# Optimization experiments

Hardware: AMD Instinct MI355X
Metric: run time of the kernel (lower is better)

## Reference

```python
import jax, jax.numpy as jnp
import numpy as np
from jax import lax

B, T, H, W, E = 64, 8, 8, 8, 512
REC = 2048


def setup_inputs() -> dict:
    key = jax.random.key(0)
    kx, kwi, kwr = jax.random.split(key, 3)
    x = jax.random.normal(kx, (B, T, H, W, E), dtype=jnp.float32)
    W_input = jax.random.normal(kwi, (E, REC), dtype=jnp.float32) / np.sqrt(E)
    W_recurrent = jax.random.normal(kwr, (REC, REC), dtype=jnp.float32) / np.sqrt(REC)
    return {"x": x, "W_input": W_input, "W_recurrent": W_recurrent}


def reference(x, W_input, W_recurrent):
    b, t, h, w, e = x.shape
    R = t * h * w
    rec = W_recurrent.shape[0]
    k = int(rec * 0.4)  # 819, matches torch: int(recurrent_size * 0.4)
    x_seq = jnp.swapaxes(x.reshape(b, R, e), 0, 1)  # [R, B, E]
    row_idx = jnp.arange(b)[:, None]

    def step(r, inp):
        z = r @ W_recurrent                    # [B, REC]
        vals, idx = lax.top_k(z, k)            # [B, k]
        s = jnp.zeros_like(z).at[row_idx, idx].set(vals)  # scatter top-k back
        r_new = jnp.tanh(inp @ W_input + s)
        r_new = r_new / (jnp.linalg.norm(r_new, axis=-1, keepdims=True) + 1e-6)
        return r_new, None

    r0 = jnp.zeros((b, rec), dtype=x.dtype)
    r_final, _ = lax.scan(step, r0, x_seq)
    return r_final
```

## Files before the change

kernel.cpp:

```cpp
#include <hip/hip_runtime.h>

#define NSTEP 512
#define EDIM  512
#define REC   2048
#define NB    64
#define KSEL  819
#define KC    8
#define ZCH   256
#define AP    264
#define CSTR  16896

typedef unsigned short u16;
typedef __bf16 bf16x8 __attribute__((ext_vector_type(8)));
typedef float  f32x4  __attribute__((ext_vector_type(4)));
typedef unsigned long long ull;

static __device__ __forceinline__ f32x4 mfma16(bf16x8 a, bf16x8 b, f32x4 c) {
    return __builtin_amdgcn_mfma_f32_16x16x32_bf16(a, b, c, 0, 0, 0);
}

static __device__ __forceinline__ void split2(float v, u16& c0, u16& c1) {
    __bf16 b0 = (__bf16)v;
    __bf16 b1 = (__bf16)(v - (float)b0);
    c0 = __builtin_bit_cast(u16, b0);
    c1 = __builtin_bit_cast(u16, b1);
}

static __device__ __forceinline__ void cstore4f(float* p, float v) {
    __hip_atomic_store((unsigned*)p, __float_as_uint(v), __ATOMIC_RELAXED, __HIP_MEMORY_SCOPE_AGENT);
}
static __device__ __forceinline__ void cstore4u(unsigned* p, unsigned v) {
    __hip_atomic_store(p, v, __ATOMIC_RELAXED, __HIP_MEMORY_SCOPE_AGENT);
}
static __device__ __forceinline__ unsigned cload4u(const unsigned* p) {
    return __hip_atomic_load(p, __ATOMIC_RELAXED, __HIP_MEMORY_SCOPE_AGENT);
}
static __device__ __forceinline__ void cstore8u(void* p, ull v) {
    __hip_atomic_store((ull*)p, v, __ATOMIC_RELAXED, __HIP_MEMORY_SCOPE_AGENT);
}
static __device__ __forceinline__ ull cload8u(const void* p) {
    return __hip_atomic_load((const ull*)p, __ATOMIC_RELAXED, __HIP_MEMORY_SCOPE_AGENT);
}
static __device__ __forceinline__ float2 cload8f(const float* p) {
    ull u = cload8u(p);
    float2 v; __builtin_memcpy(&v, &u, 8);
    return v;
}

__device__ __forceinline__ void gbarA(unsigned* bar, int bid, int tid,
                                      unsigned gen, bool wait)
{
    __syncthreads();
    if (tid == 0) cstore4u(&bar[bid], gen);
    if (bid == 0 && tid < 64) {
        const ull* sl = (const ull*)bar;
        for (;;) {
            const ull v0 = cload8u(&sl[tid * 2]);
            const ull v1 = cload8u(&sl[tid * 2 + 1]);
            const bool ok = ((unsigned)v0 >= gen) && ((unsigned)(v0 >> 32) >= gen)
                         && ((unsigned)v1 >= gen) && ((unsigned)(v1 >> 32) >= gen);
            if (__all(ok)) break;
            __builtin_amdgcn_s_sleep(1);
        }
        if (tid < 16) cstore4u(&bar[1024 + tid * 32], gen);
    }
    if (wait) {
        if (tid == 0) {
            const int g = bid >> 4;
            while (cload4u(&bar[1024 + g * 32]) < gen)
                __builtin_amdgcn_s_sleep(1);
            __asm__ volatile("" ::: "memory");
        }
        __syncthreads();
    }
}

__device__ __forceinline__ void gbarB(unsigned* bar, int bid, int tid, unsigned gen)
{
    __syncthreads();
    if (bid < NB && tid == 0) cstore4u(&bar[512 + bid], gen);
    if (bid == 0 && tid < 64) {
        for (;;) {
            const unsigned v = cload4u(&bar[512 + tid]);
            if (__all(v >= gen)) break;
            __builtin_amdgcn_s_sleep(1);
        }
        if (tid < 16) cstore4u(&bar[1536 + tid * 32], gen);
    }
    if (tid == 0) {
        const int g = bid >> 4;
        while (cload4u(&bar[1536 + g * 32]) < gen)
            __builtin_amdgcn_s_sleep(1);
        __asm__ volatile("" ::: "memory");
    }
    __syncthreads();
}

__global__ __launch_bounds__(512, 1)
void rnn_persistent(const float* __restrict__ x, const float* __restrict__ Wi,
                    const float* __restrict__ Wr, float* __restrict__ out,
                    u16* __restrict__ rTu, float* __restrict__ zb,
                    u16* __restrict__ Ybf, unsigned* __restrict__ bar)
{
    extern __shared__ __align__(16) char smem[];
    u16* WrSu = (u16*)smem;
    u16* aSu  = (u16*)(smem + 67584);
    float* WiP = (float*)smem;
    float* xP  = (float*)(smem + 16384);
    unsigned*      kS    = (unsigned*)(smem + 67584);
    unsigned char* selS  = (unsigned char*)(smem + 67584 + 8192);
    unsigned*      hist  = (unsigned*)(smem + 67584 + 10240);
    __shared__ unsigned s_byte, s_newrem, s_cnteq;
    __shared__ float red[8];

    const int bid = blockIdx.x;
    const int tid = threadIdx.x;
    const int kc = bid & 7, nc = bid >> 3;
    const int n0 = nc * 64, kcbase = kc * ZCH;
    const int wid = tid >> 6, lane = tid & 63;
    const int q = lane >> 4, l16 = lane & 15;
    const int Moff = (wid & 3) * 16, Npair = wid >> 2;
    const bool isB = (bid < NB);

    {
        const int t0 = bid * 2;
        const int tr4 = (tid >> 5) * 4;
        const int tc4 = (tid & 31) * 4;
        for (int nc2 = 0; nc2 < 16; ++nc2) {
            const int n0y = nc2 * 128;
            f32x4 acc[2][4];
#pragma unroll
            for (int h = 0; h < 2; ++h)
#pragma unroll
                for (int i = 0; i < 4; ++i) acc[h][i] = (f32x4){0,0,0,0};
            for (int kr = 0; kr < 16; ++kr) {
                const int k0y = kr * 32;
                __syncthreads();
                {
                    const int col4 = (tid & 31) * 4, row = tid >> 5;
                    *(float4*)&WiP[row * 128 + col4] =
                        *(const float4*)(Wi + (long long)(k0y + row) * REC + n0y + col4);
                    *(float4*)&WiP[(row + 16) * 128 + col4] =
                        *(const float4*)(Wi + (long long)(k0y + row + 16) * REC + n0y + col4);
                }
                for (int h = 0; h < 2; ++h) {
                    __syncthreads();
                    {
                        const int b = tid & 63, e4 = (tid >> 6) * 4;
                        const float4 v = *(const float4*)(x + ((long long)b * NSTEP + (t0 + h)) * EDIM + k0y + e4);
                        xP[(e4    ) * 64 + b] = v.x;
                        xP[(e4 + 1) * 64 + b] = v.y;
                        xP[(e4 + 2) * 64 + b] = v.z;
                        xP[(e4 + 3) * 64 + b] = v.w;
                    }
                    __syncthreads();
#pragma unroll 8
                    for (int kk = 0; kk < 32; ++kk) {
                        const float4 af = *(const float4*)&xP[kk * 64 + tr4];
                        const float4 bf = *(const float4*)&WiP[kk * 128 + tc4];
                        const float av[4] = {af.x, af.y, af.z, af.w};
#pragma unroll
                        for (int i = 0; i < 4; ++i) {
                            acc[h][i].x += av[i] * bf.x;
                            acc[h][i].y += av[i] * bf.y;
                            acc[h][i].z += av[i] * bf.z;
                            acc[h][i].w += av[i] * bf.w;
                        }
                    }
                }
            }
#pragma unroll
            for (int h = 0; h < 2; ++h)
#pragma unroll
                for (int i = 0; i < 4; ++i) {
                    const long long yrow = (long long)(t0 + h) * 64 + tr4 + i;
                    u16 o[4];
                    o[0] = __builtin_bit_cast(u16, (__bf16)acc[h][i].x);
                    o[1] = __builtin_bit_cast(u16, (__bf16)acc[h][i].y);
                    o[2] = __builtin_bit_cast(u16, (__bf16)acc[h][i].z);
                    o[3] = __builtin_bit_cast(u16, (__bf16)acc[h][i].w);
                    ull pk; __builtin_memcpy(&pk, o, 8);
                    cstore8u(&Ybf[yrow * REC + n0y + tc4], pk);
                }
        }
    }
    {
        const int g = bid * 512 + tid;
        if (g < 65536) cstore8u(rTu + (long long)g * 4, 0ull);
        cstore4f(zb + g, 0.f);
    }
    gbarA(bar, bid, tid, 1u, true);

    {
        for (int it = 0; it < 32; ++it) {
            const int row = it * 8 + wid;
            const int col = lane;
            const float v = Wr[(long long)(kcbase + row) * REC + n0 + col];
            u16 s0, s1; split2(v, s0, s1);
            const int base = col * AP + row;
            WrSu[base] = s0;
            WrSu[CSTR + base] = s1;
        }
        __syncthreads();
    }

    const int hw = tid >> 5, hl = tid & 31;
    for (int t = 0; t < NSTEP; ++t) {
        float* zcur = zb + (size_t)(t & 1) * 131072;
        float* znxt = zb + (size_t)((t + 1) & 1) * 131072;
        cstore4f(znxt + bid * 512 + tid, 0.f);
        {
            ull va[8], vbv[8];
#pragma unroll
            for (int i = 0; i < 8; ++i) {
                const int c = i >> 2;
                const int b = (i & 3) * 16 + hw;
                const u16* src = rTu + (long long)c * 131072 + (long long)b * REC + kcbase + hl * 8;
                va[i] = cload8u(src);
                vbv[i] = cload8u(src + 4);
            }
#pragma unroll
            for (int i = 0; i < 8; ++i) {
                const int c = i >> 2;
                const int b = (i & 3) * 16 + hw;
                u16* dst = aSu + c * CSTR + b * AP + hl * 8;
                *(ull*)dst = va[i];
                *(ull*)(dst + 4) = vbv[i];
            }
        }
        __syncthreads();

        f32x4 acc0 = {0,0,0,0}, acc1 = {0,0,0,0};
#pragma unroll
        for (int ks = 0; ks < 8; ++ks) {
            const int kk = ks * 32 + q * 8;
            const u16* ap = aSu + (Moff + l16) * AP + kk;
            bf16x8 A0 = *(const bf16x8*)(ap);
            bf16x8 A1 = *(const bf16x8*)(ap + CSTR);
            const u16* bp0 = WrSu + (Npair * 32 + l16) * AP + kk;
            bf16x8 B00 = *(const bf16x8*)(bp0);
            bf16x8 B01 = *(const bf16x8*)(bp0 + CSTR);
            const u16* bp1 = bp0 + 16 * AP;
            bf16x8 B10 = *(const bf16x8*)(bp1);
            bf16x8 B11 = *(const bf16x8*)(bp1 + CSTR);
            acc0 = mfma16(A0, B00, acc0);
            acc1 = mfma16(A0, B10, acc1);
            acc0 = mfma16(A0, B01, acc0);
            acc1 = mfma16(A0, B11, acc1);
            acc0 = mfma16(A1, B00, acc0);
            acc1 = mfma16(A1, B10, acc1);
        }
        {
            const int colA = n0 + Npair * 32 + l16;
#pragma unroll
            for (int i = 0; i < 4; ++i) {
                float* zp = zcur + (long long)(Moff + q * 4 + i) * REC + colA;
                unsafeAtomicAdd(zp,      ((float*)&acc0)[i]);
                unsafeAtomicAdd(zp + 16, ((float*)&acc1)[i]);
            }
        }
        gbarA(bar, bid, tid, (unsigned)(t + 2), isB);

        if (isB) {
            const int b = bid;
            const int j0 = tid * 4;
            float zs[4];
            {
                const float2 u0 = cload8f(zcur + (long long)b * REC + j0);
                const float2 u1 = cload8f(zcur + (long long)b * REC + j0 + 2);
                zs[0] = u0.x; zs[1] = u0.y; zs[2] = u1.x; zs[3] = u1.y;
            }
            const ushort4 yv = *(const ushort4*)&Ybf[((long long)t * 64 + b) * REC + j0];
            unsigned kv[4];
#pragma unroll
            for (int s = 0; s < 4; ++s) {
                const unsigned u = __float_as_uint(zs[s]);
                kv[s] = (u & 0x80000000u) ? ~u : (u | 0x80000000u);
            }
            unsigned* hw_ = hist + wid * 256;
            unsigned prefix = 0, remaining = KSEL;
            int done = 0;
            for (int byte = 3; byte >= 0 && !done; --byte) {
                {
                    uint4 zz = {0u, 0u, 0u, 0u};
                    *(uint4*)&hw_[lane * 4] = zz;
                }
                const int shift = byte * 8;
                const unsigned pmask = (byte == 3) ? 0u : (0xFFFFFFFFu << (shift + 8));
#pragma unroll
                for (int s = 0; s < 4; ++s) {
                    if ((kv[s] & pmask) == prefix)
                        atomicAdd(&hw_[(kv[s] >> shift) & 255u], 1u);
                }
                __syncthreads();
                if (tid < 64) {
                    unsigned c0 = 0, c1 = 0, c2 = 0, c3 = 0;
#pragma unroll
                    for (int w = 0; w < 8; ++w) {
                        const uint4 hv = *(const uint4*)&hist[w * 256 + tid * 4];
                        c0 += hv.x; c1 += hv.y; c2 += hv.z; c3 += hv.w;
                    }
                    const unsigned tot = c0 + c1 + c2 + c3;
                    unsigned suf = tot;
#pragma unroll
                    for (int st = 1; st < 64; st <<= 1) {
                        unsigned o = __shfl_down(suf, (unsigned)st);
                        if (tid + st >= 64) o = 0u;
                        suf += o;
                    }
                    unsigned S[5];
                    S[0] = suf; S[1] = suf - c0; S[2] = suf - c0 - c1;
                    S[3] = suf - c0 - c1 - c2; S[4] = suf - tot;
                    const unsigned cc[4] = {c0, c1, c2, c3};
#pragma unroll
                    for (int qq = 0; qq < 4; ++qq) {
                        if (S[qq] >= remaining && S[qq + 1] < remaining) {
                            s_byte = (unsigned)(tid * 4 + qq);
                            s_newrem = remaining - S[qq + 1];
                            s_cnteq = cc[qq];
                        }
                    }
                }
                __syncthreads();
                prefix |= (s_byte << shift);
                remaining = s_newrem;
                if (remaining == s_cnteq) done = 1;
            }
            unsigned char sel[4];
            if (done) {
#pragma unroll
                for (int s = 0; s < 4; ++s)
                    sel[s] = (kv[s] >= prefix) ? 1 : 0;
            } else {
                *(uint4*)&kS[j0] = *(uint4*)kv;
                __syncthreads();
                if (tid == 0) {
                    unsigned rem = remaining;
                    const unsigned T = prefix;
                    for (int j = 0; j < REC; ++j) {
                        const unsigned k = kS[j];
                        unsigned char sl = 0;
                        if (k > T) sl = 1;
                        else if (k == T && rem > 0u) { sl = 1; --rem; }
                        selS[j] = sl;
                    }
                }
                __syncthreads();
#pragma unroll
                for (int s = 0; s < 4; ++s) sel[s] = selS[j0 + s];
            }
            float rn[4]; float ss = 0.f;
            const u16 ya[4] = {yv.x, yv.y, yv.z, yv.w};
#pragma unroll
            for (int s = 0; s < 4; ++s) {
                const float y = __uint_as_float(((unsigned)ya[s]) << 16);
                const float v = y + (sel[s] ? zs[s] : 0.f);
                const float th = tanhf(v);
                rn[s] = th; ss += th * th;
            }
#pragma unroll
            for (int off = 32; off > 0; off >>= 1)
                ss += __shfl_down(ss, (unsigned)off);
            if (lane == 0) red[wid] = ss;
            __syncthreads();
            float a = 0.f;
#pragma unroll
            for (int i = 0; i < 8; ++i) a += red[i];
            const float inv = 1.0f / (sqrtf(a) + 1e-6f);
            u16 o0[4], o1[4];
            float4 ov;
#pragma unroll
            for (int s = 0; s < 4; ++s) {
                const float v = rn[s] * inv;
                split2(v, o0[s], o1[s]);
                ((float*)&ov)[s] = v;
            }
            ull p0, p1;
            __builtin_memcpy(&p0, o0, 8); __builtin_memcpy(&p1, o1, 8);
            cstore8u(rTu + (long long)b * REC + j0, p0);
            cstore8u(rTu + 131072 + (long long)b * REC + j0, p1);
            if (t == NSTEP - 1)
                *(float4*)&out[(long long)b * REC + j0] = ov;
        }
        gbarB(bar, bid, tid, (unsigned)(t + 1));
    }
}

extern "C" void kernel_launch(void* const* d_in, const int* in_sizes, int n_in,
                              void* d_out, int out_size, void* d_ws, size_t ws_size,
                              hipStream_t stream)
{
    const float* x   = (const float*)d_in[0];
    const float* Win = (const float*)d_in[1];
    const float* Wr  = (const float*)d_in[2];
    float* out = (float*)d_out;

    char* ws = (char*)d_ws;
    const size_t BAR = 8192;
    unsigned* bar = (unsigned*)ws;
    float* zb  = (float*)(ws + BAR);
    u16*   rTu = (u16*)(ws + BAR + 2 * 524288);
    u16*   Ybf = (u16*)(ws + BAR + 2 * 524288 + 524288);

    static int smem_set = 0;
    if (!smem_set) {
        hipFuncSetAttribute((const void*)rnn_persistent,
                            hipFuncAttributeMaxDynamicSharedMemorySize, 135168);
        smem_set = 1;
    }
    hipMemsetAsync(bar, 0, BAR, stream);
    rnn_persistent<<<256, 512, 135168, stream>>>(x, Win, Wr, out, rTu, zb, Ybf, bar);
}
```

Baseline: 7.594 ms.

## Use MFMA for input projection, flatten grid barriers, ballot-based top byte histogram

Computes the x@W_input prologue with split-bf16 MFMA instead of scalar FP32 FMAs, after first transposing and splitting W_input into a workspace buffer. The two-level hierarchical grid barriers are replaced by flat barriers in which every block polls all arrival flags directly. The Ybf load is issued before the barrier wait so its latency overlaps the wait. The first radix histogram pass uses wave ballots instead of LDS atomics. The extra prologue barrier and transpose add setup cost, and the flat polling puts more traffic on the barrier flags.

After: 10.21 ms. 34.5% more time.

```diff
diff --git a/kernel.cpp b/kernel.cpp
--- a/kernel.cpp
+++ b/kernel.cpp
@@ -9,6 +9,7 @@
 #define ZCH   256
 #define AP    264
 #define CSTR  16896
+#define WITC  1048576
 
 typedef unsigned short u16;
 typedef __bf16 bf16x8 __attribute__((ext_vector_type(8)));
@@ -47,66 +48,17 @@
     return v;
 }
 
-__device__ __forceinline__ void gbarA(unsigned* bar, int bid, int tid,
-                                      unsigned gen, bool wait)
-{
-    __syncthreads();
-    if (tid == 0) cstore4u(&bar[bid], gen);
-    if (bid == 0 && tid < 64) {
-        const ull* sl = (const ull*)bar;
-        for (;;) {
-            const ull v0 = cload8u(&sl[tid * 2]);
-            const ull v1 = cload8u(&sl[tid * 2 + 1]);
-            const bool ok = ((unsigned)v0 >= gen) && ((unsigned)(v0 >> 32) >= gen)
-                         && ((unsigned)v1 >= gen) && ((unsigned)(v1 >> 32) >= gen);
-            if (__all(ok)) break;
-            __builtin_amdgcn_s_sleep(1);
-        }
-        if (tid < 16) cstore4u(&bar[1024 + tid * 32], gen);
-    }
-    if (wait) {
-        if (tid == 0) {
-            const int g = bid >> 4;
-            while (cload4u(&bar[1024 + g * 32]) < gen)
-                __builtin_amdgcn_s_sleep(1);
-            __asm__ volatile("" ::: "memory");
-        }
-        __syncthreads();
-    }
-}
-
-__device__ __forceinline__ void gbarB(unsigned* bar, int bid, int tid, unsigned gen)
-{
-    __syncthreads();
-    if (bid < NB && tid == 0) cstore4u(&bar[512 + bid], gen);
-    if (bid == 0 && tid < 64) {
-        for (;;) {
-            const unsigned v = cload4u(&bar[512 + tid]);
-            if (__all(v >= gen)) break;
-            __builtin_amdgcn_s_sleep(1);
-        }
-        if (tid < 16) cstore4u(&bar[1536 + tid * 32], gen);
-    }
-    if (tid == 0) {
-        const int g = bid >> 4;
-        while (cload4u(&bar[1536 + g * 32]) < gen)
-            __builtin_amdgcn_s_sleep(1);
-        __asm__ volatile("" ::: "memory");
-    }
-    __syncthreads();
-}
-
 __global__ __launch_bounds__(512, 1)
 void rnn_persistent(const float* __restrict__ x, const float* __restrict__ Wi,
                     const float* __restrict__ Wr, float* __restrict__ out,
                     u16* __restrict__ rTu, float* __restrict__ zb,
-                    u16* __restrict__ Ybf, unsigned* __restrict__ bar)
+                    u16* __restrict__ Ybf, u16* __restrict__ WiTu,
+                    unsigned* __restrict__ bar)
 {
     extern __shared__ __align__(16) char smem[];
     u16* WrSu = (u16*)smem;
     u16* aSu  = (u16*)(smem + 67584);
-    float* WiP = (float*)smem;
-    float* xP  = (float*)(smem + 16384);
+    float* tp = (float*)smem;
     unsigned*      kS    = (unsigned*)(smem + 67584);
     unsigned char* selS  = (unsigned char*)(smem + 67584 + 8192);
     unsigned*      hist  = (unsigned*)(smem + 67584 + 10240);
@@ -123,64 +75,113 @@
     const bool isB = (bid < NB);
 
     {
+        const int jt = bid & 31, et = bid >> 5;
+        const int j0 = jt * 64, e0 = et * 64;
+        const int rr = tid >> 6, ln = tid & 63;
+#pragma unroll
+        for (int k = 0; k < 8; ++k) {
+            const int r = k * 8 + rr;
+            tp[r * 65 + ln] = Wi[(long long)(e0 + r) * REC + j0 + ln];
+        }
+        __syncthreads();
+        const int c = tid >> 3, e8 = (tid & 7) * 8;
+        u16 h[8], l[8];
+#pragma unroll
+        for (int i = 0; i < 8; ++i) split2(tp[(e8 + i) * 65 + c], h[i], l[i]);
+        ull ph0, ph1, pl0, pl1;
+        __builtin_memcpy(&ph0, &h[0], 8); __builtin_memcpy(&ph1, &h[4], 8);
+        __builtin_memcpy(&pl0, &l[0], 8); __builtin_memcpy(&pl1, &l[4], 8);
+        const long long bI = (long long)(j0 + c) * 512 + e0 + e8;
+        cstore8u(&WiTu[bI], ph0);        cstore8u(&WiTu[bI + 4], ph1);
+        cstore8u(&WiTu[WITC + bI], pl0); cstore8u(&WiTu[WITC + bI + 4], pl1);
+    }
+    __syncthreads();
+    if (tid == 0) cstore4u(&bar[bid], 1u);
+    if (tid < 256) { while (cload4u(&bar[tid]) < 1u) __builtin_amdgcn_s_sleep(1); }
+    __asm__ volatile("" ::: "memory");
+    __syncthreads();
+
+    {
         const int t0 = bid * 2;
-        const int tr4 = (tid >> 5) * 4;
-        const int tc4 = (tid & 31) * 4;
-        for (int nc2 = 0; nc2 < 16; ++nc2) {
-            const int n0y = nc2 * 128;
-            f32x4 acc[2][4];
-#pragma unroll
-            for (int h = 0; h < 2; ++h)
-#pragma unroll
-                for (int i = 0; i < 4; ++i) acc[h][i] = (f32x4){0,0,0,0};
-            for (int kr = 0; kr < 16; ++kr) {
-                const int k0y = kr * 32;
+        for (int jc = 0; jc < 32; ++jc) {
+            const int j0y = jc * 64;
+            f32x4 aY[2][2];
+#pragma unroll
+            for (int tt = 0; tt < 2; ++tt)
+#pragma unroll
+                for (int i = 0; i < 2; ++i) aY[tt][i] = (f32x4){0,0,0,0};
+            for (int kc2 = 0; kc2 < 2; ++kc2) {
                 __syncthreads();
-                {
-                    const int col4 = (tid & 31) * 4, row = tid >> 5;
-                    *(float4*)&WiP[row * 128 + col4] =
-                        *(const float4*)(Wi + (long long)(k0y + row) * REC + n0y + col4);
-                    *(float4*)&WiP[(row + 16) * 128 + col4] =
-                        *(const float4*)(Wi + (long long)(k0y + row + 16) * REC + n0y + col4);
-                }
-                for (int h = 0; h < 2; ++h) {
+#pragma unroll
+                for (int i = 0; i < 8; ++i) {
+                    const int chunk = i * 512 + tid;
+                    const int cc = chunk >> 11;
+                    const int jj = (chunk & 2047) >> 5;
+                    const int e8 = chunk & 31;
+                    const u16* src = WiTu + (long long)cc * WITC
+                                   + (long long)(j0y + jj) * 512 + kc2 * 256 + e8 * 8;
+                    const ull w0 = *(const ull*)src;
+                    const ull w1 = *(const ull*)(src + 4);
+                    u16* dst = WrSu + cc * CSTR + jj * AP + e8 * 8;
+                    *(ull*)dst = w0;
+                    *(ull*)(dst + 4) = w1;
+                }
+#pragma unroll
+                for (int tt = 0; tt < 2; ++tt) {
                     __syncthreads();
-                    {
-                        const int b = tid & 63, e4 = (tid >> 6) * 4;
-                        const float4 v = *(const float4*)(x + ((long long)b * NSTEP + (t0 + h)) * EDIM + k0y + e4);
-                        xP[(e4    ) * 64 + b] = v.x;
-                        xP[(e4 + 1) * 64 + b] = v.y;
-                        xP[(e4 + 2) * 64 + b] = v.z;
-                        xP[(e4 + 3) * 64 + b] = v.w;
+#pragma unroll
+                    for (int it = 0; it < 8; ++it) {
+                        const int b = it * 8 + wid;
+                        const float4 v = *(const float4*)(x
+                            + ((long long)b * NSTEP + (t0 + tt)) * EDIM
+                            + kc2 * 256 + lane * 4);
+                        u16 hh[4], ll[4];
+                        split2(v.x, hh[0], ll[0]); split2(v.y, hh[1], ll[1]);
+                        split2(v.z, hh[2], ll[2]); split2(v.w, hh[3], ll[3]);
+                        ull ph, pl;
+                        __builtin_memcpy(&ph, hh, 8); __builtin_memcpy(&pl, ll, 8);
+                        *(ull*)&aSu[b * AP + lane * 4] = ph;
+                        *(ull*)&aSu[CSTR + b * AP + lane * 4] = pl;
                     }
                     __syncthreads();
-#pragma unroll 8
-                    for (int kk = 0; kk < 32; ++kk) {
-                        const float4 af = *(const float4*)&xP[kk * 64 + tr4];
-                        const float4 bf = *(const float4*)&WiP[kk * 128 + tc4];
-                        const float av[4] = {af.x, af.y, af.z, af.w};
-#pragma unroll
-                        for (int i = 0; i < 4; ++i) {
-                            acc[h][i].x += av[i] * bf.x;
-                            acc[h][i].y += av[i] * bf.y;
-                            acc[h][i].z += av[i] * bf.z;
-                            acc[h][i].w += av[i] * bf.w;
-                        }
-                    }
-                }
-            }
-#pragma unroll
-            for (int h = 0; h < 2; ++h)
+                    f32x4 a0 = aY[tt][0], a1 = aY[tt][1];
+#pragma unroll
+                    for (int ks = 0; ks < 8; ++ks) {
+                        const int kk = ks * 32 + q * 8;
+                        const u16* ap = aSu + (Moff + l16) * AP + kk;
+                        bf16x8 A0 = *(const bf16x8*)(ap);
+                        bf16x8 A1 = *(const bf16x8*)(ap + CSTR);
+                        const u16* bp0 = WrSu + (Npair * 32 + l16) * AP + kk;
+                        bf16x8 B00 = *(const bf16x8*)(bp0);
+                        bf16x8 B01 = *(const bf16x8*)(bp0 + CSTR);
+                        const u16* bp1 = bp0 + 16 * AP;
+                        bf16x8 B10 = *(const bf16x8*)(bp1);
+                        bf16x8 B11 = *(const bf16x8*)(bp1 + CSTR);
+                        a0 = mfma16(A0, B00, a0);
+                        a1 = mfma16(A0, B10, a1);
+                        a0 = mfma16(A0, B01, a0);
+                        a1 = mfma16(A0, B11, a1);
+                        a0 = mfma16(A1, B00, a0);
+                        a1 = mfma16(A1, B10, a1);
+                    }
+                    aY[tt][0] = a0; aY[tt][1] = a1;
+                }
+            }
+            const int jb = j0y + Npair * 32 + l16;
+#pragma unroll
+            for (int tt = 0; tt < 2; ++tt)
 #pragma unroll
                 for (int i = 0; i < 4; ++i) {
-                    const long long yrow = (long long)(t0 + h) * 64 + tr4 + i;
-                    u16 o[4];
-                    o[0] = __builtin_bit_cast(u16, (__bf16)acc[h][i].x);
-                    o[1] = __builtin_bit_cast(u16, (__bf16)acc[h][i].y);
-                    o[2] = __builtin_bit_cast(u16, (__bf16)acc[h][i].z);
-                    o[3] = __builtin_bit_cast(u16, (__bf16)acc[h][i].w);
-                    ull pk; __builtin_memcpy(&pk, o, 8);
-                    cstore8u(&Ybf[yrow * REC + n0y + tc4], pk);
+                    const int row = Moff + q * 4 + i;
+                    const unsigned w0 = (unsigned)__builtin_bit_cast(u16, (__bf16)((float*)&aY[tt][0])[i]);
+                    const unsigned w1 = (unsigned)__builtin_bit_cast(u16, (__bf16)((float*)&aY[tt][1])[i]);
+                    const unsigned o0 = (unsigned)__shfl_xor((int)w0, 1);
+                    const unsigned o1 = (unsigned)__shfl_xor((int)w1, 1);
+                    if ((lane & 1) == 0) {
+                        const long long yb = ((long long)(t0 + tt) * 64 + row) * REC + jb;
+                        cstore4u((unsigned*)&Ybf[yb],      w0 | (o0 << 16));
+                        cstore4u((unsigned*)&Ybf[yb + 16], w1 | (o1 << 16));
+                    }
                 }
         }
     }
@@ -189,7 +190,11 @@
         if (g < 65536) cstore8u(rTu + (long long)g * 4, 0ull);
         cstore4f(zb + g, 0.f);
     }
-    gbarA(bar, bid, tid, 1u, true);
+    __syncthreads();
+    if (tid == 0) cstore4u(&bar[bid], 2u);
+    if (tid < 256) { while (cload4u(&bar[tid]) < 2u) __builtin_amdgcn_s_sleep(1); }
+    __asm__ volatile("" ::: "memory");
+    __syncthreads();
 
     {
         for (int it = 0; it < 32; ++it) {
@@ -259,18 +264,25 @@
                 unsafeAtomicAdd(zp + 16, ((float*)&acc1)[i]);
             }
         }
-        gbarA(bar, bid, tid, (unsigned)(t + 2), isB);
+        __syncthreads();
+        if (tid == 0) cstore4u(&bar[bid], (unsigned)(t + 3));
 
         if (isB) {
             const int b = bid;
             const int j0 = tid * 4;
+            const ushort4 yv = *(const ushort4*)&Ybf[((long long)t * 64 + b) * REC + j0];
+            if (tid < 256) {
+                while (cload4u(&bar[tid]) < (unsigned)(t + 3)) __builtin_amdgcn_s_sleep(1);
+            }
+            __asm__ volatile("" ::: "memory");
+            __syncthreads();
+
             float zs[4];
             {
                 const float2 u0 = cload8f(zcur + (long long)b * REC + j0);
                 const float2 u1 = cload8f(zcur + (long long)b * REC + j0 + 2);
                 zs[0] = u0.x; zs[1] = u0.y; zs[2] = u1.x; zs[3] = u1.y;
             }
-            const ushort4 yv = *(const ushort4*)&Ybf[((long long)t * 64 + b) * REC + j0];
             unsigned kv[4];
 #pragma unroll
             for (int s = 0; s < 4; ++s) {
@@ -286,11 +298,28 @@
                     *(uint4*)&hw_[lane * 4] = zz;
                 }
                 const int shift = byte * 8;
-                const unsigned pmask = (byte == 3) ? 0u : (0xFFFFFFFFu << (shift + 8));
-#pragma unroll
-                for (int s = 0; s < 4; ++s) {
-                    if ((kv[s] & pmask) == prefix)
-                        atomicAdd(&hw_[(kv[s] >> shift) & 255u], 1u);
+                if (byte == 3) {
+                    unsigned bbs[4];
+#pragma unroll
+                    for (int s = 0; s < 4; ++s) bbs[s] = kv[s] >> 24;
+#pragma unroll
+                    for (int s = 0; s < 4; ++s) {
+                        ull rem = ~0ull;
+                        while (rem) {
+                            const int src = (int)__ffsll((unsigned long long)rem) - 1;
+                            const unsigned v = (unsigned)__shfl((int)bbs[s], src);
+                            const ull eq = __ballot(bbs[s] == v);
+                            if ((int)lane == src) hw_[v] += (unsigned)__popcll(eq);
+                            rem &= ~eq;
+                        }
+                    }
+                } else {
+                    const unsigned pmask = 0xFFFFFFFFu << (shift + 8);
+#pragma unroll
+                    for (int s = 0; s < 4; ++s) {
+                        if ((kv[s] & pmask) == prefix)
+                            atomicAdd(&hw_[(kv[s] >> shift) & 255u], 1u);
+                    }
                 }
                 __syncthreads();
                 if (tid < 64) {
@@ -382,7 +411,14 @@
             if (t == NSTEP - 1)
                 *(float4*)&out[(long long)b * REC + j0] = ov;
         }
-        gbarB(bar, bid, tid, (unsigned)(t + 1));
+
+        __syncthreads();
+        if (isB && tid == 0) cstore4u(&bar[512 + bid], (unsigned)(t + 1));
+        if (tid < 64) {
+            while (cload4u(&bar[512 + tid]) < (unsigned)(t + 1)) __builtin_amdgcn_s_sleep(1);
+        }
+        __asm__ volatile("" ::: "memory");
+        __syncthreads();
     }
 }
 
@@ -397,10 +433,11 @@
 
     char* ws = (char*)d_ws;
     const size_t BAR = 8192;
-    unsigned* bar = (unsigned*)ws;
-    float* zb  = (float*)(ws + BAR);
-    u16*   rTu = (u16*)(ws + BAR + 2 * 524288);
-    u16*   Ybf = (u16*)(ws + BAR + 2 * 524288 + 524288);
+    unsigned* bar  = (unsigned*)ws;
+    float*    zb   = (float*)(ws + BAR);
+    u16*      rTu  = (u16*)(ws + BAR + 2 * 524288);
+    u16*      WiTu = (u16*)(ws + BAR + 2 * 524288 + 524288);
+    u16*      Ybf  = (u16*)(ws + BAR + 2 * 524288 + 524288 + 4194304);
 
     static int smem_set = 0;
     if (!smem_set) {
@@ -409,5 +446,5 @@
         smem_set = 1;
     }
     hipMemsetAsync(bar, 0, BAR, stream);
-    rnn_persistent<<<256, 512, 135168, stream>>>(x, Win, Wr, out, rTu, zb, Ybf, bar);
-}
+    rnn_persistent<<<256, 512, 135168, stream>>>(x, Win, Wr, out, rTu, zb, Ybf, WiTu, bar);
+}
```
